# Optimization experiments

Measured on AMD Instinct MI355X. Metric: run time of the kernel, lower is better.

## Reference

```python
import jax, jax.numpy as jnp
import numpy as np


def _batch_conv2d(inputs, kernels):
    # inputs: [B, 1, H, W], kernels: [B, 1, 3, 3]; distinct kernel per sample
    # Implemented as a grouped conv: view inputs as [1, B, H, W], groups=B.
    B, _, H, W = inputs.shape
    out = jax.lax.conv_general_dilated(
        inputs.reshape(1, B, H, W),
        kernels,  # OIHW with O=B, I=1
        window_strides=(1, 1),
        padding=((1, 1), (1, 1)),
        feature_group_count=B,
        dimension_numbers=("NCHW", "OIHW", "NCHW"),
    )
    return out.reshape(B, 1, H, W)


def setup_inputs() -> dict:
    key = jax.random.key(0)
    k1, k2, k3 = jax.random.split(key, 3)
    B, m = 64, 512
    x = jax.random.normal(k1, (B, 1, m, m), dtype=jnp.float32)
    f = jax.random.normal(k2, (B, 1, m, m), dtype=jnp.float32)
    kernelA = jax.random.normal(k3, (B, 1, 3, 3), dtype=jnp.float32)
    return {"x": x, "f": f, "kernelA": kernelA}


def reference(x, f, kernelA):
    # One Jacobi-style smoothing step: x <- x + (f - A x) / 6
    Ax = _batch_conv2d(x, kernelA)
    x = x + (f - Ax) * (1.0 / 6.0)
    return x
```

## Files before the change

kernel.cpp:

```cpp
#include <hip/hip_runtime.h>

#define BB 64
#define HH 512
#define WW 512
#define W4 (WW / 4)

__global__ __launch_bounds__(256) void jacobi_step_kernel(
    const float* __restrict__ x,
    const float* __restrict__ f,
    const float* __restrict__ k,
    float* __restrict__ out)
{
    const int t  = blockIdx.x * 256 + threadIdx.x;
    const int j4 = t & (W4 - 1);
    const int i  = (t >> 7) & (HH - 1);
    const int b  = t >> 16;
    if (b >= BB) return;

    const float*  xb  = x + (size_t)b * HH * WW;
    const float4* xb4 = (const float4*)xb;
    const float*  kb  = k + b * 9;

    const float k00 = kb[0], k01 = kb[1], k02 = kb[2];
    const float k10 = kb[3], k11 = kb[4], k12 = kb[5];
    const float k20 = kb[6], k21 = kb[7], k22 = kb[8];

    const int j0 = j4 << 2;
    const bool has_l = (j0 > 0);
    const bool has_r = (j0 + 4 < WW);

    const float4 vc = xb4[i * W4 + j4];
    const float  lc = has_l ? xb[i * WW + j0 - 1] : 0.f;
    const float  rc = has_r ? xb[i * WW + j0 + 4] : 0.f;

    float4 vm = make_float4(0.f, 0.f, 0.f, 0.f);
    float  lm = 0.f, rm = 0.f;
    if (i > 0) {
        vm = xb4[(i - 1) * W4 + j4];
        lm = has_l ? xb[(i - 1) * WW + j0 - 1] : 0.f;
        rm = has_r ? xb[(i - 1) * WW + j0 + 4] : 0.f;
    }

    float4 vp = make_float4(0.f, 0.f, 0.f, 0.f);
    float  lp = 0.f, rp = 0.f;
    if (i < HH - 1) {
        vp = xb4[(i + 1) * W4 + j4];
        lp = has_l ? xb[(i + 1) * WW + j0 - 1] : 0.f;
        rp = has_r ? xb[(i + 1) * WW + j0 + 4] : 0.f;
    }

    float4 acc;
    acc.x = k00 * lm   + k01 * vm.x + k02 * vm.y
          + k10 * lc   + k11 * vc.x + k12 * vc.y
          + k20 * lp   + k21 * vp.x + k22 * vp.y;
    acc.y = k00 * vm.x + k01 * vm.y + k02 * vm.z
          + k10 * vc.x + k11 * vc.y + k12 * vc.z
          + k20 * vp.x + k21 * vp.y + k22 * vp.z;
    acc.z = k00 * vm.y + k01 * vm.z + k02 * vm.w
          + k10 * vc.y + k11 * vc.z + k12 * vc.w
          + k20 * vp.y + k21 * vp.z + k22 * vp.w;
    acc.w = k00 * vm.z + k01 * vm.w + k02 * rm
          + k10 * vc.z + k11 * vc.w + k12 * rc
          + k20 * vp.z + k21 * vp.w + k22 * rp;

    const size_t idx4 = (size_t)b * HH * W4 + (size_t)i * W4 + j4;
    const float4 fv = ((const float4*)f)[idx4];

    const float inv6 = 1.f / 6.f;
    float4 o;
    o.x = vc.x + (fv.x - acc.x) * inv6;
    o.y = vc.y + (fv.y - acc.y) * inv6;
    o.z = vc.z + (fv.z - acc.z) * inv6;
    o.w = vc.w + (fv.w - acc.w) * inv6;

    ((float4*)out)[idx4] = o;
}

extern "C" void kernel_launch(void* const* d_in, const int* in_sizes, int n_in,
                              void* d_out, int out_size, void* d_ws, size_t ws_size,
                              hipStream_t stream) {
    const float* x = (const float*)d_in[0];
    const float* f = (const float*)d_in[1];
    const float* k = (const float*)d_in[2];
    float* out = (float*)d_out;

    const int total_quads = BB * HH * W4;
    const int blocks = (total_quads + 255) / 256;
    jacobi_step_kernel<<<blocks, 256, 0, stream>>>(x, f, k, out);
}
```

Before: 174.6 us.

## March each wavefront down rows with register-resident stencil rows

Each wavefront now processes 8 consecutive rows of one image, with each lane covering 8 columns. The three stencil rows are kept in registers and shifted as it marches downward. This removes the threefold reloading of x rows that the one-quad-per-thread version relied on cache for, and it reduces thread count and index overhead. In exchange there is less parallelism per launch, and the per-lane memory accesses are wider and strided, which may coalesce less well.

Result: slower. 180.4 us (+3.3%).

```diff
diff --git a/kernel.cpp b/kernel.cpp
--- a/kernel.cpp
+++ b/kernel.cpp
@@ -3,77 +3,93 @@
 #define BB 64
 #define HH 512
 #define WW 512
-#define W4 (WW / 4)
+#define P  8
 
-__global__ __launch_bounds__(256) void jacobi_step_kernel(
+
+struct Ext { float e[10]; };
+
+__device__ __forceinline__ Ext load_ext_row(const float* __restrict__ xrow,
+                                            int c0, int lane) {
+    Ext r;
+    const float4 q0 = *(const float4*)(xrow + c0);
+    const float4 q1 = *(const float4*)(xrow + c0 + 4);
+    r.e[1] = q0.x; r.e[2] = q0.y; r.e[3] = q0.z; r.e[4] = q0.w;
+    r.e[5] = q1.x; r.e[6] = q1.y; r.e[7] = q1.z; r.e[8] = q1.w;
+    r.e[0] = (lane > 0)  ? xrow[c0 - 1] : 0.f;
+    r.e[9] = (lane < 63) ? xrow[c0 + 8] : 0.f;
+    return r;
+}
+
+__device__ __forceinline__ Ext zero_ext() {
+    Ext r;
+#pragma unroll
+    for (int j = 0; j < 10; ++j) r.e[j] = 0.f;
+    return r;
+}
+
+__global__ __launch_bounds__(256) void jacobi_march_kernel(
     const float* __restrict__ x,
     const float* __restrict__ f,
     const float* __restrict__ k,
     float* __restrict__ out)
 {
-    const int t  = blockIdx.x * 256 + threadIdx.x;
-    const int j4 = t & (W4 - 1);
-    const int i  = (t >> 7) & (HH - 1);
-    const int b  = t >> 16;
-    if (b >= BB) return;
+    const int lane = threadIdx.x & 63;
+    const int wv   = threadIdx.x >> 6;
 
-    const float*  xb  = x + (size_t)b * HH * WW;
-    const float4* xb4 = (const float4*)xb;
-    const float*  kb  = k + b * 9;
+    int S = blockIdx.x * 4 + wv;
+    S = __builtin_amdgcn_readfirstlane(S);
+    const int g  = S & 63;
+    const int b  = S >> 6;
+    const int r0 = g * P;
+    const int c0 = lane << 3;
 
+    const size_t img = (size_t)b * HH * WW;
+    const float* xb = x + img;
+    const float* fb = f + img;
+    float*       ob = out + img;
+
+    const float* kb = k + b * 9;
     const float k00 = kb[0], k01 = kb[1], k02 = kb[2];
     const float k10 = kb[3], k11 = kb[4], k12 = kb[5];
     const float k20 = kb[6], k21 = kb[7], k22 = kb[8];
 
-    const int j0 = j4 << 2;
-    const bool has_l = (j0 > 0);
-    const bool has_r = (j0 + 4 < WW);
-
-    const float4 vc = xb4[i * W4 + j4];
-    const float  lc = has_l ? xb[i * WW + j0 - 1] : 0.f;
-    const float  rc = has_r ? xb[i * WW + j0 + 4] : 0.f;
-
-    float4 vm = make_float4(0.f, 0.f, 0.f, 0.f);
-    float  lm = 0.f, rm = 0.f;
-    if (i > 0) {
-        vm = xb4[(i - 1) * W4 + j4];
-        lm = has_l ? xb[(i - 1) * WW + j0 - 1] : 0.f;
-        rm = has_r ? xb[(i - 1) * WW + j0 + 4] : 0.f;
-    }
-
-    float4 vp = make_float4(0.f, 0.f, 0.f, 0.f);
-    float  lp = 0.f, rp = 0.f;
-    if (i < HH - 1) {
-        vp = xb4[(i + 1) * W4 + j4];
-        lp = has_l ? xb[(i + 1) * WW + j0 - 1] : 0.f;
-        rp = has_r ? xb[(i + 1) * WW + j0 + 4] : 0.f;
-    }
-
-    float4 acc;
-    acc.x = k00 * lm   + k01 * vm.x + k02 * vm.y
-          + k10 * lc   + k11 * vc.x + k12 * vc.y
-          + k20 * lp   + k21 * vp.x + k22 * vp.y;
-    acc.y = k00 * vm.x + k01 * vm.y + k02 * vm.z
-          + k10 * vc.x + k11 * vc.y + k12 * vc.z
-          + k20 * vp.x + k21 * vp.y + k22 * vp.z;
-    acc.z = k00 * vm.y + k01 * vm.z + k02 * vm.w
-          + k10 * vc.y + k11 * vc.z + k12 * vc.w
-          + k20 * vp.y + k21 * vp.z + k22 * vp.w;
-    acc.w = k00 * vm.z + k01 * vm.w + k02 * rm
-          + k10 * vc.z + k11 * vc.w + k12 * rc
-          + k20 * vp.z + k21 * vp.w + k22 * rp;
-
-    const size_t idx4 = (size_t)b * HH * W4 + (size_t)i * W4 + j4;
-    const float4 fv = ((const float4*)f)[idx4];
+    Ext m, c, p;
+    m = (r0 > 0) ? load_ext_row(xb + (size_t)(r0 - 1) * WW, c0, lane)
+                 : zero_ext();
+    c = load_ext_row(xb + (size_t)r0 * WW, c0, lane);
 
     const float inv6 = 1.f / 6.f;
-    float4 o;
-    o.x = vc.x + (fv.x - acc.x) * inv6;
-    o.y = vc.y + (fv.y - acc.y) * inv6;
-    o.z = vc.z + (fv.z - acc.z) * inv6;
-    o.w = vc.w + (fv.w - acc.w) * inv6;
 
-    ((float4*)out)[idx4] = o;
+#pragma unroll
+    for (int ii = 0; ii < P; ++ii) {
+        const int i = r0 + ii;
+        p = (i + 1 < HH) ? load_ext_row(xb + (size_t)(i + 1) * WW, c0, lane)
+                         : zero_ext();
+
+        const float* frow = fb + (size_t)i * WW + c0;
+        const float4 f0 = *(const float4*)(frow);
+        const float4 f1 = *(const float4*)(frow + 4);
+
+        float o[8];
+#pragma unroll
+        for (int j = 0; j < 8; ++j) {
+            float acc = k00 * m.e[j] + k01 * m.e[j + 1] + k02 * m.e[j + 2]
+                      + k10 * c.e[j] + k11 * c.e[j + 1] + k12 * c.e[j + 2]
+                      + k20 * p.e[j] + k21 * p.e[j + 1] + k22 * p.e[j + 2];
+            const float fv = (j < 4) ? ((const float*)&f0)[j]
+                                     : ((const float*)&f1)[j - 4];
+            o[j] = c.e[j + 1] + (fv - acc) * inv6;
+        }
+
+        float* orow = ob + (size_t)i * WW + c0;
+        float4 o0 = make_float4(o[0], o[1], o[2], o[3]);
+        float4 o1 = make_float4(o[4], o[5], o[6], o[7]);
+        *(float4*)(orow)     = o0;
+        *(float4*)(orow + 4) = o1;
+
+        m = c;
+        c = p;
+    }
 }
 
 extern "C" void kernel_launch(void* const* d_in, const int* in_sizes, int n_in,
@@ -84,7 +100,6 @@
     const float* k = (const float*)d_in[2];
     float* out = (float*)d_out;
 
-    const int total_quads = BB * HH * W4;
-    const int blocks = (total_quads + 255) / 256;
-    jacobi_step_kernel<<<blocks, 256, 0, stream>>>(x, f, k, out);
+    const int blocks = (BB * (HH / P)) / 4;
+    jacobi_march_kernel<<<blocks, 256, 0, stream>>>(x, f, k, out);
 }
```
